# Kernel tuning notes

Measured on AMD Instinct MI355X. Metric: run time of the kernel, lower is better.

The kernel has to match this reference:

```python
import jax, jax.numpy as jnp
import numpy as np

V, E, HID, K, S = 100000, 256, 512, 20, 4096
HD = HID // 2  # per-direction LSTM hidden
START_ID, STOP_ID = 18, 19


def setup_inputs() -> dict:
    key = jax.random.key(0)
    ks = jax.random.split(key, 14)
    sentence = jax.random.randint(ks[0], (S,), 0, V)
    tags = jax.random.randint(ks[1], (S,), 0, START_ID)  # real tags only
    embed = jax.random.normal(ks[2], (V, E), jnp.float32) * 0.1
    w_ih_f = jax.random.normal(ks[3], (4 * HD, E), jnp.float32) * 0.05
    w_hh_f = jax.random.normal(ks[4], (4 * HD, HD), jnp.float32) * 0.05
    b_f = jax.random.normal(ks[5], (4 * HD,), jnp.float32) * 0.05
    w_ih_b = jax.random.normal(ks[6], (4 * HD, E), jnp.float32) * 0.05
    w_hh_b = jax.random.normal(ks[7], (4 * HD, HD), jnp.float32) * 0.05
    b_b = jax.random.normal(ks[8], (4 * HD,), jnp.float32) * 0.05
    h0 = jax.random.normal(ks[9], (2, HD), jnp.float32)
    c0 = jax.random.normal(ks[10], (2, HD), jnp.float32)
    emit_W = jax.random.normal(ks[11], (K, HID), jnp.float32) * 0.05
    emit_b = jax.random.normal(ks[12], (K,), jnp.float32) * 0.05
    transition = jax.random.normal(ks[13], (K, K), jnp.float32)
    transition = transition.at[START_ID, :].set(-10000.0)
    transition = transition.at[:, STOP_ID].set(-10000.0)
    return dict(sentence=sentence, tags=tags, embed=embed,
                w_ih_f=w_ih_f, w_hh_f=w_hh_f, b_f=b_f,
                w_ih_b=w_ih_b, w_hh_b=w_hh_b, b_b=b_b,
                h0=h0, c0=c0, emit_W=emit_W, emit_b=emit_b,
                transition=transition)


def _lstm_scan(xs, w_ih, w_hh, b, h, c):
    # xs: (S, E); torch gate order i, f, g, o
    def step(carry, x):
        h, c = carry
        z = x @ w_ih.T + h @ w_hh.T + b  # (4*HD,)
        i, f, g, o = jnp.split(z, 4)
        i, f, o = jax.nn.sigmoid(i), jax.nn.sigmoid(f), jax.nn.sigmoid(o)
        g = jnp.tanh(g)
        c = f * c + i * g
        h = o * jnp.tanh(c)
        return (h, c), h
    _, hs = jax.lax.scan(step, (h, c), xs)
    return hs  # (S, HD)


def reference(sentence, tags, embed, w_ih_f, w_hh_f, b_f,
              w_ih_b, w_hh_b, b_b, h0, c0, emit_W, emit_b, transition):
    xs = embed[sentence]  # (S, E)
    h_fwd = _lstm_scan(xs, w_ih_f, w_hh_f, b_f, h0[0], c0[0])
    h_bwd = _lstm_scan(xs[::-1], w_ih_b, w_hh_b, b_b, h0[1], c0[1])[::-1]
    feats = jnp.concatenate([h_fwd, h_bwd], axis=-1) @ emit_W.T + emit_b  # (S, K)

    # CRF forward algorithm (log-partition), tag dim fully vectorized.
    init_fv = jnp.full((K,), -10000.0, feats.dtype).at[START_ID].set(0.0)

    def crf_step(fv, feat):
        # fv_new[next] = logsumexp_prev(fv[prev] + T[next, prev] + feat[next])
        fv = jax.scipy.special.logsumexp(fv[None, :] + transition + feat[:, None], axis=1)
        return fv, None

    fv, _ = jax.lax.scan(crf_step, init_fv, feats)
    log_z = jax.scipy.special.logsumexp(fv + transition[STOP_ID])

    # Gold path score.
    tags_ext = jnp.concatenate([jnp.array([START_ID], tags.dtype), tags])
    gold = (transition[tags_ext[1:], tags_ext[:-1]].sum()
            + feats[jnp.arange(S), tags].sum()
            + transition[STOP_ID, tags[-1]])
    return jnp.stack([log_z, gold])
```

## Files before the change

kernel.cpp:

```cpp
#include <hip/hip_runtime.h>
#include <stdint.h>

#define SLEN 4096
#define EDIM 256
#define HD 256
#define G4 1024
#define KT 20
#define START_ID 18
#define STOP_ID 19

#define NVC 23
#define NLC 9
#define LSTM_LDS_BYTES (1024 + 1024 * NLC * 16)

typedef _Float16 half_t;
typedef _Float16 half2_t __attribute__((ext_vector_type(2)));

__device__ __forceinline__ float dot2(uint32_t w, uint32_t h, float acc) {
#if __has_builtin(__builtin_amdgcn_fdot2)
    return __builtin_amdgcn_fdot2(__builtin_bit_cast(half2_t, w),
                                  __builtin_bit_cast(half2_t, h), acc, false);
#else
    half2_t wv = __builtin_bit_cast(half2_t, w);
    half2_t hv = __builtin_bit_cast(half2_t, h);
    acc += (float)wv.x * (float)hv.x;
    acc += (float)wv.y * (float)hv.y;
    return acc;
#endif
}

__device__ __forceinline__ float fsig(float x) { return 1.f / (1.f + __expf(-x)); }
__device__ __forceinline__ float ftanh(float x) { return 1.f - 2.f / (__expf(2.f * x) + 1.f); }


__global__ __launch_bounds__(256) void k_transpose_ih(const float* __restrict__ wf,
                                                      const float* __restrict__ wb,
                                                      float* __restrict__ wT) {
    __shared__ float tile[32][33];
    int d = blockIdx.z;
    const float* w = d ? wb : wf;
    int ob = blockIdx.x * 32;
    int eb = blockIdx.y * 32;
    int tx = threadIdx.x & 31, ty = threadIdx.x >> 5;
#pragma unroll
    for (int r = 0; r < 32; r += 8)
        tile[ty + r][tx] = w[(long)(ob + ty + r) * EDIM + eb + tx];
    __syncthreads();
    float* dst = wT + (long)d * EDIM * G4;
#pragma unroll
    for (int r = 0; r < 32; r += 8)
        dst[(long)(eb + ty + r) * G4 + ob + tx] = tile[tx][ty + r];
}

__global__ __launch_bounds__(1024) void k_pack_hh(const float* __restrict__ whf,
                                                  const float* __restrict__ whb,
                                                  uint32_t* __restrict__ wpack,
                                                  uint32_t* __restrict__ wtail) {
    int d = blockIdx.y;
    const float* W = d ? whb : whf;
    int t = threadIdx.x;
    int wv = t >> 6, l = t & 63;
    int j = (wv << 4) | (l & 15);
    int g = (l >> 4) & 3;
    int o = g * 256 + j;
    int bx = blockIdx.x;
    if (bx < 92) {
        int k = bx * 2;
        half2_t p = {(half_t)W[(long)o * HD + k], (half_t)W[(long)o * HD + k + 1]};
        wpack[(d * 92 + bx) * 1024 + t] = __builtin_bit_cast(uint32_t, p);
    } else {
        int cb = bx - 92;
        uint32_t q[4];
#pragma unroll
        for (int qq = 0; qq < 4; qq++) {
            int k = 2 * (92 + cb * 4 + qq);
            half2_t p = {(half_t)W[(long)o * HD + k], (half_t)W[(long)o * HD + k + 1]};
            q[qq] = __builtin_bit_cast(uint32_t, p);
        }
        uint4* dst = (uint4*)wtail;
        dst[(d * NLC + cb) * 1024 + t] = make_uint4(q[0], q[1], q[2], q[3]);
    }
}

__global__ __launch_bounds__(256) void k_zx(const int* __restrict__ sentence,
                                            const float* __restrict__ embed,
                                            const float* __restrict__ wT,
                                            const float* __restrict__ bf,
                                            const float* __restrict__ bb,
                                            float* __restrict__ zxp) {
    int d = blockIdx.y;
    int s0 = blockIdx.x * 16;
    const float* bias = d ? bb : bf;
    __shared__ float xbuf[16][EDIM];
    int tid = threadIdx.x;
    for (int r = 0; r < 16; r++) {
        int row = sentence[s0 + r];
        xbuf[r][tid] = embed[(long)row * EDIM + tid];
    }
    __syncthreads();
    const float* wTd = wT + (long)d * EDIM * G4;
    for (int og = 0; og < 4; og++) {
        float acc[16];
#pragma unroll
        for (int r = 0; r < 16; r++) acc[r] = 0.f;
        int o = og * 256 + tid;
        for (int e = 0; e < EDIM; e += 4) {
            float w0 = wTd[(long)(e + 0) * G4 + o];
            float w1 = wTd[(long)(e + 1) * G4 + o];
            float w2 = wTd[(long)(e + 2) * G4 + o];
            float w3 = wTd[(long)(e + 3) * G4 + o];
#pragma unroll
            for (int r = 0; r < 16; r++) {
                float4 x4 = *(const float4*)&xbuf[r][e];
                acc[r] += w0 * x4.x + w1 * x4.y + w2 * x4.z + w3 * x4.w;
            }
        }
        float bv = bias[o];
        int tB = ((tid >> 4) << 6) | (og << 4) | (tid & 15);
#pragma unroll
        for (int r = 0; r < 16; r++)
            zxp[(long)(d * SLEN + s0 + r) * G4 + tB] = acc[r] + bv;
    }
}

__global__ __launch_bounds__(1024)
__attribute__((amdgpu_waves_per_eu(4, 4)))
void k_lstm(const float* __restrict__ zxp,
            const uint32_t* __restrict__ wpack,
            const uint4* __restrict__ wtail,
            const float* __restrict__ h0,
            const float* __restrict__ c0,
            float* __restrict__ hs) {
    extern __shared__ char smem[];
    uint4* h2q = (uint4*)smem;
    half_t* h2h = (half_t*)smem;
    uint4* tail = (uint4*)(smem + 1024);

    int d = blockIdx.x;
    int t = threadIdx.x;
    int l = t & 63;
    int j = ((t >> 6) << 4) | (l & 15);

    uint32_t wreg[4 * NVC];
#pragma unroll
    for (int kk = 0; kk < 4 * NVC; kk++) wreg[kk] = wpack[(d * 92 + kk) * 1024 + t];
#pragma unroll
    for (int kk = 0; kk < 4 * NVC; kk++) asm volatile("" : "+v"(wreg[kk]));

#pragma unroll
    for (int cb = 0; cb < NLC; cb++)
        tail[cb * 1024 + t] = wtail[(d * NLC + cb) * 1024 + t];

    float c = c0[d * HD + j];
    if (t < 128) {
        half2_t p = {(half_t)h0[d * HD + 2 * t], (half_t)h0[d * HD + 2 * t + 1]};
        ((uint32_t*)h2q)[t] = __builtin_bit_cast(uint32_t, p);
    }
    __syncthreads();

    const float* zxd = zxp + (long)d * SLEN * G4 + t;
    float* hsd = hs + (long)d * SLEN * HD + j;

    float zx_next = zxd[(long)(d ? SLEN - 1 : 0) * G4];

    for (int s = 0; s < SLEN; s++) {
        const int p = s & 1;
        float zx = zx_next;
        if (s + 1 < SLEN) {
            int sxn = d ? (SLEN - 2 - s) : (s + 1);
            zx_next = zxd[(long)sxn * G4];
        }
        const uint4* hq = h2q + p * 32;
        float acc0 = 0.f, acc1 = 0.f;
#pragma unroll
        for (int cc = 0; cc < NVC; cc++) {
            uint4 hv = hq[cc];
            acc0 = dot2(wreg[4 * cc + 0], hv.x, acc0);
            acc1 = dot2(wreg[4 * cc + 1], hv.y, acc1);
            acc0 = dot2(wreg[4 * cc + 2], hv.z, acc0);
            acc1 = dot2(wreg[4 * cc + 3], hv.w, acc1);
        }
#pragma unroll
        for (int cb = 0; cb < NLC; cb++) {
            uint4 tw = tail[cb * 1024 + t];
            uint4 hv = hq[NVC + cb];
            acc0 = dot2(tw.x, hv.x, acc0);
            acc1 = dot2(tw.y, hv.y, acc1);
            acc0 = dot2(tw.z, hv.z, acc0);
            acc1 = dot2(tw.w, hv.w, acc1);
        }
        float z = acc0 + acc1 + zx;
        int lj = l & 15;
        float zi = __shfl(z, lj, 64);
        float zf = __shfl(z, lj + 16, 64);
        float zg = __shfl(z, lj + 32, 64);
        float zo = __shfl(z, lj + 48, 64);
        float ig = fsig(zi), fg = fsig(zf), og = fsig(zo);
        float gg = ftanh(zg);
        c = fg * c + ig * gg;
        float hval = og * ftanh(c);
        if (l < 16) {
            int sx = d ? (SLEN - 1 - s) : s;
            hsd[(long)sx * HD] = hval;
            h2h[((p ^ 1) << 8) + j] = (half_t)hval;
        }
        __syncthreads();
    }
}

__global__ __launch_bounds__(192) void k_feats(const float* __restrict__ hs,
                                               const float* __restrict__ emitW,
                                               const float* __restrict__ emitb,
                                               float* __restrict__ feats) {
    __shared__ float wb[KT][516];
    __shared__ float hb[8][516];
    int tid = threadIdx.x;
    int s0 = blockIdx.x * 8;
    for (int idx = tid; idx < KT * 512; idx += 192) {
        wb[idx >> 9][idx & 511] = emitW[idx];
    }
    for (int idx = tid; idx < 8 * 512; idx += 192) {
        int sl = idx >> 9, jj = idx & 511;
        float v = (jj < 256) ? hs[(long)(s0 + sl) * HD + jj]
                             : hs[(long)(SLEN + s0 + sl) * HD + (jj - 256)];
        hb[sl][jj] = v;
    }
    __syncthreads();
    if (tid < 160) {
        int sl = tid / KT, k = tid % KT;
        float acc = emitb[k];
        for (int jj = 0; jj < 512; jj += 4) {
            float4 wv = *(const float4*)&wb[k][jj];
            float4 hv = *(const float4*)&hb[sl][jj];
            acc += wv.x * hv.x + wv.y * hv.y + wv.z * hv.z + wv.w * hv.w;
        }
        feats[(long)(s0 + sl) * KT + k] = acc;
    }
}

__global__ __launch_bounds__(256) void k_gold(const float* __restrict__ feats,
                                              const int* __restrict__ tags,
                                              const float* __restrict__ trans,
                                              float* __restrict__ out) {
    __shared__ float red[256];
    int tid = threadIdx.x;
    float local = 0.f;
    for (int s2 = tid; s2 < SLEN; s2 += 256) {
        int cur = tags[s2];
        int prev = s2 ? tags[s2 - 1] : START_ID;
        local += trans[cur * KT + prev] + feats[(long)s2 * KT + cur];
    }
    red[tid] = local;
    __syncthreads();
    for (int off = 128; off; off >>= 1) {
        if (tid < off) red[tid] += red[tid + off];
        __syncthreads();
    }
    if (tid == 0) out[1] = red[0] + trans[STOP_ID * KT + tags[SLEN - 1]];
}

__global__ __launch_bounds__(512) void k_crf_chunk(const float* __restrict__ feats,
                                                   const float* __restrict__ trans,
                                                   float* __restrict__ mats) {
    __shared__ float T[KT][KT + 1];
    __shared__ float fb[16][KT];
    __shared__ float cur[2][KT][KT + 1];
    int tid = threadIdx.x;
    int t0 = blockIdx.x * 16;
    if (tid < KT * KT) T[tid / KT][tid % KT] = trans[tid];
    for (int idx = tid; idx < 16 * KT; idx += 512) fb[idx / KT][idx % KT] = feats[(long)t0 * KT + idx];
    __syncthreads();
    int i = tid / KT, jc = tid % KT;
    bool act = tid < KT * KT;
    if (act) cur[0][i][jc] = T[i][jc] + fb[0][i];
    __syncthreads();
    for (int m = 1; m < 16; m++) {
        int p = (m - 1) & 1;
        float nv = 0.f;
        if (act) {
            float vs[KT], vmax = -1e30f;
#pragma unroll
            for (int k = 0; k < KT; k++) { vs[k] = T[i][k] + cur[p][k][jc]; vmax = fmaxf(vmax, vs[k]); }
            float sum = 0.f;
#pragma unroll
            for (int k = 0; k < KT; k++) sum += __expf(vs[k] - vmax);
            nv = fb[m][i] + vmax + __logf(sum);
        }
        if (act) cur[p ^ 1][i][jc] = nv;
        __syncthreads();
    }
    if (act) mats[(long)blockIdx.x * (KT * KT) + tid] = cur[1][i][jc];
}

__global__ __launch_bounds__(512) void k_crf_combine(const float* __restrict__ in,
                                                     float* __restrict__ out_mats,
                                                     int per_block,
                                                     const float* __restrict__ trans,
                                                     float* __restrict__ d_out_ptr,
                                                     int finalize) {
    __shared__ float A[KT][KT + 1];
    __shared__ float cur[2][KT][KT + 1];
    int tid = threadIdx.x;
    int b = blockIdx.x;
    int i = tid / KT, jc = tid % KT;
    bool act = tid < KT * KT;
    const float* base = in + (long)b * per_block * (KT * KT);
    if (act) cur[0][i][jc] = base[tid];
    __syncthreads();
    for (int m = 1; m < per_block; m++) {
        int p = (m - 1) & 1;
        if (act) A[i][jc] = base[(long)m * KT * KT + tid];
        __syncthreads();
        float nv = 0.f;
        if (act) {
            float vs[KT], vmax = -1e30f;
#pragma unroll
            for (int k = 0; k < KT; k++) { vs[k] = A[i][k] + cur[p][k][jc]; vmax = fmaxf(vmax, vs[k]); }
            float sum = 0.f;
#pragma unroll
            for (int k = 0; k < KT; k++) sum += __expf(vs[k] - vmax);
            nv = vmax + __logf(sum);
        }
        if (act) cur[p ^ 1][i][jc] = nv;
        __syncthreads();
    }
    int fbuf = (per_block - 1) & 1;
    if (!finalize) {
        if (act) out_mats[(long)b * KT * KT + tid] = cur[fbuf][i][jc];
        return;
    }
    if (tid == 0) {
        float fv[KT];
        for (int ii = 0; ii < KT; ii++) {
            float vs[KT], vmax = -1e30f;
            for (int k = 0; k < KT; k++) {
                float v = cur[fbuf][ii][k] + (k == START_ID ? 0.f : -10000.f);
                vs[k] = v;
                vmax = fmaxf(vmax, v);
            }
            float sum = 0.f;
            for (int k = 0; k < KT; k++) sum += __expf(vs[k] - vmax);
            fv[ii] = vmax + __logf(sum);
        }
        float vs2[KT], vmax = -1e30f;
        for (int ii = 0; ii < KT; ii++) {
            float v = fv[ii] + trans[STOP_ID * KT + ii];
            vs2[ii] = v;
            vmax = fmaxf(vmax, v);
        }
        float sum = 0.f;
        for (int ii = 0; ii < KT; ii++) sum += __expf(vs2[ii] - vmax);
        d_out_ptr[0] = vmax + __logf(sum);
    }
}

extern "C" void kernel_launch(void* const* d_in, const int* in_sizes, int n_in,
                              void* d_out, int out_size, void* d_ws, size_t ws_size,
                              hipStream_t stream) {
    const int* sentence = (const int*)d_in[0];
    const int* tags = (const int*)d_in[1];
    const float* embed = (const float*)d_in[2];
    const float* w_ih_f = (const float*)d_in[3];
    const float* w_hh_f = (const float*)d_in[4];
    const float* b_f = (const float*)d_in[5];
    const float* w_ih_b = (const float*)d_in[6];
    const float* w_hh_b = (const float*)d_in[7];
    const float* b_b = (const float*)d_in[8];
    const float* h0 = (const float*)d_in[9];
    const float* c0 = (const float*)d_in[10];
    const float* emit_W = (const float*)d_in[11];
    const float* emit_b = (const float*)d_in[12];
    const float* transition = (const float*)d_in[13];
    float* out = (float*)d_out;

    char* ws = (char*)d_ws;
    float* zxp = (float*)(ws + 0);
    float* hs = (float*)(ws + 33554432);
    float* wT = (float*)(ws + 41943040);
    uint32_t* wpack = (uint32_t*)(ws + 44040192);
    uint32_t* wtail = (uint32_t*)(ws + 44793856);
    float* feats = (float*)(ws + 45088768);
    float* mats = (float*)(ws + 45416448);
    float* mats2 = (float*)(ws + 45826048);

    (void)hipFuncSetAttribute((const void*)k_lstm,
                              hipFuncAttributeMaxDynamicSharedMemorySize,
                              LSTM_LDS_BYTES);

    k_transpose_ih<<<dim3(32, 8, 2), 256, 0, stream>>>(w_ih_f, w_ih_b, wT);
    k_pack_hh<<<dim3(101, 2), 1024, 0, stream>>>(w_hh_f, w_hh_b, wpack, wtail);
    k_zx<<<dim3(256, 2), 256, 0, stream>>>(sentence, embed, wT, b_f, b_b, zxp);
    k_lstm<<<dim3(2), 1024, LSTM_LDS_BYTES, stream>>>(zxp, wpack, (const uint4*)wtail, h0, c0, hs);
    k_feats<<<dim3(512), 192, 0, stream>>>(hs, emit_W, emit_b, feats);
    k_gold<<<dim3(1), 256, 0, stream>>>(feats, tags, transition, out);
    k_crf_chunk<<<dim3(256), 512, 0, stream>>>(feats, transition, mats);
    k_crf_combine<<<dim3(16), 512, 0, stream>>>(mats, mats2, 16, transition, out, 0);
    k_crf_combine<<<dim3(1), 512, 0, stream>>>(mats2, nullptr, 16, transition, out, 1);
}
```

Measured before the change: 9.169 ms.

## Halve LSTM block to 512 threads, two gate rows per thread, readlane h broadcast

The recurrent LSTM kernel now runs 512 threads per direction, and each thread computes two gate rows (i/f and g/o pairs) from 208 register-resident fp16 weight pairs plus a smaller LDS tail. Hidden-state values are loaded once per wave from LDS and broadcast with readlane, replacing per-thread uint4 LDS reads. The weight packing and zx layout are changed to match. The aim is to shorten the per-step barrier and cut LDS traffic on the serial critical path. In exchange, register pressure rises sharply (waves_per_eu 2) and each thread does twice the serial dot-product work.

```diff
diff --git a/kernel.cpp b/kernel.cpp
--- a/kernel.cpp
+++ b/kernel.cpp
@@ -9,9 +9,9 @@
 #define START_ID 18
 #define STOP_ID 19
 
-#define NVC 23
-#define NLC 9
-#define LSTM_LDS_BYTES (1024 + 1024 * NLC * 16)
+#define NVW 104
+#define NTC 6
+#define LSTM_LDS_BYTES (1024 + 512 * 2 * NTC * 16)
 
 typedef _Float16 half_t;
 typedef _Float16 half2_t __attribute__((ext_vector_type(2)));
@@ -29,9 +29,16 @@
 #endif
 }
 
+__device__ __forceinline__ uint32_t rdlane(uint32_t v, int lane) {
+#if __has_builtin(__builtin_amdgcn_readlane)
+    return (uint32_t)__builtin_amdgcn_readlane((int)v, lane);
+#else
+    return (uint32_t)__shfl((int)v, lane, 64);
+#endif
+}
+
 __device__ __forceinline__ float fsig(float x) { return 1.f / (1.f + __expf(-x)); }
 __device__ __forceinline__ float ftanh(float x) { return 1.f - 2.f / (__expf(2.f * x) + 1.f); }
-
 
 __global__ __launch_bounds__(256) void k_transpose_ih(const float* __restrict__ wf,
                                                       const float* __restrict__ wb,
@@ -52,33 +59,39 @@
         dst[(long)(eb + ty + r) * G4 + ob + tx] = tile[tx][ty + r];
 }
 
-__global__ __launch_bounds__(1024) void k_pack_hh(const float* __restrict__ whf,
-                                                  const float* __restrict__ whb,
-                                                  uint32_t* __restrict__ wpack,
-                                                  uint32_t* __restrict__ wtail) {
+__global__ __launch_bounds__(512) void k_pack_hh(const float* __restrict__ whf,
+                                                 const float* __restrict__ whb,
+                                                 uint32_t* __restrict__ wpack,
+                                                 uint32_t* __restrict__ wtail) {
     int d = blockIdx.y;
     const float* W = d ? whb : whf;
     int t = threadIdx.x;
-    int wv = t >> 6, l = t & 63;
-    int j = (wv << 4) | (l & 15);
-    int g = (l >> 4) & 3;
-    int o = g * 256 + j;
+    int w = t >> 6, l = t & 63;
+    int jj = l & 31, p = (l >> 5) & 1;
+    int j = 32 * w + jj;
+    int rowA = j + 256 * p;
+    int rowB = j + 512 + 256 * p;
     int bx = blockIdx.x;
-    if (bx < 92) {
-        int k = bx * 2;
-        half2_t p = {(half_t)W[(long)o * HD + k], (half_t)W[(long)o * HD + k + 1]};
-        wpack[(d * 92 + bx) * 1024 + t] = __builtin_bit_cast(uint32_t, p);
+    if (bx < 2 * NVW) {
+        int m = bx;
+        int row = (m < NVW) ? rowA : rowB;
+        int k2 = (m < NVW) ? m : m - NVW;
+        half2_t pk = {(half_t)W[(long)row * HD + 2 * k2],
+                      (half_t)W[(long)row * HD + 2 * k2 + 1]};
+        wpack[(d * 2 * NVW + m) * 512 + t] = __builtin_bit_cast(uint32_t, pk);
     } else {
-        int cb = bx - 92;
+        int c = bx - 2 * NVW;
+        int row = (c < NTC) ? rowA : rowB;
+        int base = NVW + 4 * ((c < NTC) ? c : c - NTC);
         uint32_t q[4];
 #pragma unroll
         for (int qq = 0; qq < 4; qq++) {
-            int k = 2 * (92 + cb * 4 + qq);
-            half2_t p = {(half_t)W[(long)o * HD + k], (half_t)W[(long)o * HD + k + 1]};
-            q[qq] = __builtin_bit_cast(uint32_t, p);
-        }
-        uint4* dst = (uint4*)wtail;
-        dst[(d * NLC + cb) * 1024 + t] = make_uint4(q[0], q[1], q[2], q[3]);
+            int k2 = base + qq;
+            half2_t pk = {(half_t)W[(long)row * HD + 2 * k2],
+                          (half_t)W[(long)row * HD + 2 * k2 + 1]};
+            q[qq] = __builtin_bit_cast(uint32_t, pk);
+        }
+        ((uint4*)wtail)[(d * 2 * NTC + c) * 512 + t] = make_uint4(q[0], q[1], q[2], q[3]);
     }
 }
 
@@ -116,15 +129,16 @@
             }
         }
         float bv = bias[o];
-        int tB = ((tid >> 4) << 6) | (og << 4) | (tid & 15);
+        int base = ((tid >> 5) << 6) + (tid & 31);
+        int q = base + 32 * (og & 1) + 512 * (og >> 1);
 #pragma unroll
         for (int r = 0; r < 16; r++)
-            zxp[(long)(d * SLEN + s0 + r) * G4 + tB] = acc[r] + bv;
-    }
-}
-
-__global__ __launch_bounds__(1024)
-__attribute__((amdgpu_waves_per_eu(4, 4)))
+            zxp[(long)(d * SLEN + s0 + r) * G4 + q] = acc[r] + bv;
+    }
+}
+
+__global__ __launch_bounds__(512)
+__attribute__((amdgpu_waves_per_eu(2, 2)))
 void k_lstm(const float* __restrict__ zxp,
             const uint32_t* __restrict__ wpack,
             const uint4* __restrict__ wtail,
@@ -132,74 +146,82 @@
             const float* __restrict__ c0,
             float* __restrict__ hs) {
     extern __shared__ char smem[];
-    uint4* h2q = (uint4*)smem;
     half_t* h2h = (half_t*)smem;
     uint4* tail = (uint4*)(smem + 1024);
 
     int d = blockIdx.x;
     int t = threadIdx.x;
-    int l = t & 63;
-    int j = ((t >> 6) << 4) | (l & 15);
-
-    uint32_t wreg[4 * NVC];
-#pragma unroll
-    for (int kk = 0; kk < 4 * NVC; kk++) wreg[kk] = wpack[(d * 92 + kk) * 1024 + t];
-#pragma unroll
-    for (int kk = 0; kk < 4 * NVC; kk++) asm volatile("" : "+v"(wreg[kk]));
-
-#pragma unroll
-    for (int cb = 0; cb < NLC; cb++)
-        tail[cb * 1024 + t] = wtail[(d * NLC + cb) * 1024 + t];
-
-    float c = c0[d * HD + j];
+    int w = t >> 6, l = t & 63;
+    int jj = l & 31;
+    int j = 32 * w + jj;
+
+    uint32_t wreg[2 * NVW];
+#pragma unroll
+    for (int m = 0; m < 2 * NVW; m++) wreg[m] = wpack[(d * 2 * NVW + m) * 512 + t];
+#pragma unroll
+    for (int m = 0; m < 2 * NVW; m++) asm volatile("" : "+v"(wreg[m]));
+
+#pragma unroll
+    for (int c = 0; c < 2 * NTC; c++)
+        tail[c * 512 + t] = wtail[(d * 2 * NTC + c) * 512 + t];
+
+    float cst = c0[d * HD + j];
     if (t < 128) {
-        half2_t p = {(half_t)h0[d * HD + 2 * t], (half_t)h0[d * HD + 2 * t + 1]};
-        ((uint32_t*)h2q)[t] = __builtin_bit_cast(uint32_t, p);
-    }
-    __syncthreads();
-
-    const float* zxd = zxp + (long)d * SLEN * G4 + t;
+        half2_t pk = {(half_t)h0[d * HD + 2 * t], (half_t)h0[d * HD + 2 * t + 1]};
+        ((uint32_t*)smem)[t] = __builtin_bit_cast(uint32_t, pk);
+    }
+    __syncthreads();
+
+    const float* zxd = zxp + (long)d * SLEN * G4;
     float* hsd = hs + (long)d * SLEN * HD + j;
 
-    float zx_next = zxd[(long)(d ? SLEN - 1 : 0) * G4];
+    int sx0 = d ? SLEN - 1 : 0;
+    float zxa_n = zxd[(long)sx0 * G4 + t];
+    float zxb_n = zxd[(long)sx0 * G4 + 512 + t];
 
     for (int s = 0; s < SLEN; s++) {
         const int p = s & 1;
-        float zx = zx_next;
+        float zxa = zxa_n, zxb = zxb_n;
         if (s + 1 < SLEN) {
             int sxn = d ? (SLEN - 2 - s) : (s + 1);
-            zx_next = zxd[(long)sxn * G4];
-        }
-        const uint4* hq = h2q + p * 32;
-        float acc0 = 0.f, acc1 = 0.f;
-#pragma unroll
-        for (int cc = 0; cc < NVC; cc++) {
-            uint4 hv = hq[cc];
-            acc0 = dot2(wreg[4 * cc + 0], hv.x, acc0);
-            acc1 = dot2(wreg[4 * cc + 1], hv.y, acc1);
-            acc0 = dot2(wreg[4 * cc + 2], hv.z, acc0);
-            acc1 = dot2(wreg[4 * cc + 3], hv.w, acc1);
-        }
-#pragma unroll
-        for (int cb = 0; cb < NLC; cb++) {
-            uint4 tw = tail[cb * 1024 + t];
-            uint4 hv = hq[NVC + cb];
-            acc0 = dot2(tw.x, hv.x, acc0);
-            acc1 = dot2(tw.y, hv.y, acc1);
-            acc0 = dot2(tw.z, hv.z, acc0);
-            acc1 = dot2(tw.w, hv.w, acc1);
-        }
-        float z = acc0 + acc1 + zx;
-        int lj = l & 15;
-        float zi = __shfl(z, lj, 64);
-        float zf = __shfl(z, lj + 16, 64);
-        float zg = __shfl(z, lj + 32, 64);
-        float zo = __shfl(z, lj + 48, 64);
+            zxa_n = zxd[(long)sxn * G4 + t];
+            zxb_n = zxd[(long)sxn * G4 + 512 + t];
+        }
+        uint2 hv = ((const uint2*)(smem + p * 512))[l];
+        uint32_t hr0 = hv.x, hr1 = hv.y;
+
+        float a0 = 0.f, a1 = 0.f;
+#pragma unroll
+        for (int m = 0; m < NVW; m++) {
+            uint32_t hdw = rdlane((m & 1) ? hr1 : hr0, m >> 1);
+            a0 = dot2(wreg[m], hdw, a0);
+            a1 = dot2(wreg[NVW + m], hdw, a1);
+        }
+#pragma unroll
+        for (int c = 0; c < NTC; c++) {
+            uint4 ta = tail[c * 512 + t];
+            uint4 tb = tail[(NTC + c) * 512 + t];
+#pragma unroll
+            for (int q = 0; q < 4; q++) {
+                int m = NVW + 4 * c + q;
+                uint32_t hdw = rdlane((m & 1) ? hr1 : hr0, m >> 1);
+                uint32_t wa = (q == 0) ? ta.x : (q == 1) ? ta.y : (q == 2) ? ta.z : ta.w;
+                uint32_t wb = (q == 0) ? tb.x : (q == 1) ? tb.y : (q == 2) ? tb.z : tb.w;
+                a0 = dot2(wa, hdw, a0);
+                a1 = dot2(wb, hdw, a1);
+            }
+        }
+        float z0 = a0 + zxa;
+        float z1 = a1 + zxb;
+        float zi = __shfl(z0, jj, 64);
+        float zf = __shfl(z0, jj + 32, 64);
+        float zg = __shfl(z1, jj, 64);
+        float zo = __shfl(z1, jj + 32, 64);
         float ig = fsig(zi), fg = fsig(zf), og = fsig(zo);
         float gg = ftanh(zg);
-        c = fg * c + ig * gg;
-        float hval = og * ftanh(c);
-        if (l < 16) {
+        cst = fg * cst + ig * gg;
+        float hval = og * ftanh(cst);
+        if (l < 32) {
             int sx = d ? (SLEN - 1 - s) : s;
             hsd[(long)sx * HD] = hval;
             h2h[((p ^ 1) << 8) + j] = (half_t)hval;
@@ -378,7 +400,7 @@
     float* hs = (float*)(ws + 33554432);
     float* wT = (float*)(ws + 41943040);
     uint32_t* wpack = (uint32_t*)(ws + 44040192);
-    uint32_t* wtail = (uint32_t*)(ws + 44793856);
+    uint32_t* wtail = (uint32_t*)(ws + 44892160);
     float* feats = (float*)(ws + 45088768);
     float* mats = (float*)(ws + 45416448);
     float* mats2 = (float*)(ws + 45826048);
@@ -388,9 +410,9 @@
                               LSTM_LDS_BYTES);
 
     k_transpose_ih<<<dim3(32, 8, 2), 256, 0, stream>>>(w_ih_f, w_ih_b, wT);
-    k_pack_hh<<<dim3(101, 2), 1024, 0, stream>>>(w_hh_f, w_hh_b, wpack, wtail);
+    k_pack_hh<<<dim3(220, 2), 512, 0, stream>>>(w_hh_f, w_hh_b, wpack, wtail);
     k_zx<<<dim3(256, 2), 256, 0, stream>>>(sentence, embed, wT, b_f, b_b, zxp);
-    k_lstm<<<dim3(2), 1024, LSTM_LDS_BYTES, stream>>>(zxp, wpack, (const uint4*)wtail, h0, c0, hs);
+    k_lstm<<<dim3(2), 512, LSTM_LDS_BYTES, stream>>>(zxp, wpack, (const uint4*)wtail, h0, c0, hs);
     k_feats<<<dim3(512), 192, 0, stream>>>(hs, emit_W, emit_b, feats);
     k_gold<<<dim3(1), 256, 0, stream>>>(feats, tags, transition, out);
     k_crf_chunk<<<dim3(256), 512, 0, stream>>>(feats, transition, mats);
```

New measurement: 9.044 ms. No clear change (-1.4%).
